# Performance work log

Measured on AMD Instinct MI355X. Metric: run time of the kernel, lower is better.

The kernel has to match this reference:

```python
import jax, jax.numpy as jnp
import numpy as np

OBS, HOR, PD, HID, NH, PROTO = 8, 8, 128, 256, 8, 32
B, N = 8, 4096

def _gelu(x):
    return jax.nn.gelu(x, approximate=False)  # torch nn.GELU default is exact erf

def setup_inputs():
    key = jax.random.key(0)
    ks = iter(jax.random.split(key, 40))
    nrm = lambda shape, s=0.02: jax.random.normal(next(ks), shape, dtype=jnp.float32) * s
    return {
        'obs_points': jax.random.normal(next(ks), (B, N, OBS, 2), dtype=jnp.float32),
        'obs_vis': jax.random.randint(next(ks), (B, N, OBS), 0, 2).astype(bool),
        'rel_xy': jax.random.normal(next(ks), (B, N, 2), dtype=jnp.float32),
        'anchor_obs': jax.random.normal(next(ks), (B, OBS, 2), dtype=jnp.float32),
        'anchor_obs_vel': jax.random.normal(next(ks), (B, OBS, 2), dtype=jnp.float32),
        'semantic_feat': jax.random.normal(next(ks), (B, N, 10), dtype=jnp.float32),
        'ln_w': jnp.ones((OBS * 7,), jnp.float32),
        'ln_b': jnp.zeros((OBS * 7,), jnp.float32),
        'enc_w1': nrm((OBS * 7, PD)), 'enc_b1': jnp.zeros((PD,), jnp.float32),
        'enc_w2': nrm((PD, PD)), 'enc_b2': jnp.zeros((PD,), jnp.float32),
        'time_embed': nrm((HOR, HID)),
        'anchor_w': nrm((OBS * 4, HID)), 'anchor_b': jnp.zeros((HID,), jnp.float32),
        'query_w': nrm((PD, HID)), 'query_b': jnp.zeros((HID,), jnp.float32),
        'in_proj_w': nrm((HID, 3 * HID)), 'in_proj_b': jnp.zeros((3 * HID,), jnp.float32),
        'out_proj_w': nrm((HID, HID)), 'out_proj_b': jnp.zeros((HID,), jnp.float32),
        'ah_w': nrm((HID, 2)), 'ah_b': jnp.zeros((2,), jnp.float32),
        'rh_w1': nrm((HID + PD + 2, HID)), 'rh_b1': jnp.zeros((HID,), jnp.float32),
        'rh_w2': nrm((HID, 2)), 'rh_b2': jnp.zeros((2,), jnp.float32),
        'vh_w1': nrm((HID + PD, HID // 2)), 'vh_b1': jnp.zeros((HID // 2,), jnp.float32),
        'vh_w2': nrm((HID // 2, 1)), 'vh_b2': jnp.zeros((1,), jnp.float32),
        'sh_w': nrm((HID, PROTO)), 'sh_b': jnp.zeros((PROTO,), jnp.float32),
    }

def reference(obs_points, obs_vis, rel_xy, anchor_obs, anchor_obs_vel, semantic_feat,
              ln_w, ln_b, enc_w1, enc_b1, enc_w2, enc_b2, time_embed,
              anchor_w, anchor_b, query_w, query_b, in_proj_w, in_proj_b,
              out_proj_w, out_proj_b, ah_w, ah_b, rh_w1, rh_b1, rh_w2, rh_b2,
              vh_w1, vh_b1, vh_w2, vh_b2, sh_w, sh_b):
    del semantic_feat  # unused, matches original
    Bc, Nc, T, _ = obs_points.shape
    # ---- PointTraceEncoder ----
    vel = jnp.concatenate([jnp.zeros_like(obs_points[:, :, :1]),
                           obs_points[:, :, 1:] - obs_points[:, :, :-1]], axis=2)
    rel = jnp.broadcast_to(rel_xy[:, :, None, :], (Bc, Nc, T, 2))
    feat = jnp.concatenate([obs_points, vel, obs_vis.astype(jnp.float32)[..., None], rel],
                           axis=-1).reshape(Bc, Nc, T * 7)
    mu = feat.mean(-1, keepdims=True)
    var = ((feat - mu) ** 2).mean(-1, keepdims=True)
    x = (feat - mu) / jnp.sqrt(var + 1e-5) * ln_w + ln_b
    point_tokens = _gelu(_gelu(x @ enc_w1 + enc_b1) @ enc_w2 + enc_b2)  # [B,N,PD]
    # ---- queries / memory ----
    anchor_feat = jnp.concatenate([anchor_obs, anchor_obs_vel], -1).reshape(Bc, -1)
    tq = time_embed[None] + (anchor_feat @ anchor_w + anchor_b)[:, None]  # [B,HOR,HID]
    mem = point_tokens @ query_w + query_b  # [B,N,HID]
    # ---- multi-head cross attention ----
    D = tq.shape[-1]; dh = D // NH
    q = tq @ in_proj_w[:, :D] + in_proj_b[:D]
    k = mem @ in_proj_w[:, D:2 * D] + in_proj_b[D:2 * D]
    v = mem @ in_proj_w[:, 2 * D:] + in_proj_b[2 * D:]
    qh = q.reshape(Bc, -1, NH, dh).transpose(0, 2, 1, 3)
    kh = k.reshape(Bc, -1, NH, dh).transpose(0, 2, 1, 3)
    vh = v.reshape(Bc, -1, NH, dh).transpose(0, 2, 1, 3)
    attn = jax.nn.softmax(jnp.einsum('bhqd,bhkd->bhqk', qh, kh) / jnp.sqrt(jnp.float32(dh)), axis=-1)
    o = jnp.einsum('bhqk,bhkd->bhqd', attn, vh).transpose(0, 2, 1, 3).reshape(Bc, -1, D)
    future = o @ out_proj_w + out_proj_b  # [B,HOR,HID]
    # ---- heads ----
    last_anchor = anchor_obs[:, -1]
    anchor_delta = 0.1 * jnp.tanh(future @ ah_w + ah_b)
    anchor_pred = last_anchor[:, None] + jnp.cumsum(anchor_delta, axis=1)  # [B,HOR,2]
    Hq = future.shape[1]
    ft_e = jnp.broadcast_to(future[:, :, None, :], (Bc, Hq, Nc, D))
    pt_e = jnp.broadcast_to(point_tokens[:, None], (Bc, Hq, Nc, point_tokens.shape[-1]))
    rel_e = jnp.broadcast_to(rel_xy[:, None], (Bc, Hq, Nc, 2))
    per_point = jnp.concatenate([ft_e, pt_e, rel_e], axis=-1)  # [B,HOR,N,HID+PD+2]
    residual = 0.1 * jnp.tanh(_gelu(per_point @ rh_w1 + rh_b1) @ rh_w2 + rh_b2)
    pred_points = anchor_pred[:, :, None, :] + residual
    vis_logits = (_gelu(per_point[..., :-2] @ vh_w1 + vh_b1) @ vh_w2 + vh_b2)[..., 0]
    sem_logits = future @ sh_w + sh_b
    return (anchor_pred,
            pred_points.transpose(0, 2, 1, 3),   # [B,N,HOR,2]
            vis_logits.transpose(0, 2, 1),       # [B,N,HOR]
            sem_logits)                           # [B,HOR,PROTO]
```

## Files before the change

kernel.cpp:

```cpp
#include <hip/hip_runtime.h>
#include <math.h>

#define BB 8
#define NN 4096
#define TT 8
#define HORQ 8
#define PD 128
#define HID 256
#define NHD 8
#define DH 32
#define FE 56
#define NC 8
#define CH 512

typedef __attribute__((ext_vector_type(8))) short short8;
typedef __attribute__((ext_vector_type(4))) float floatx4;

__device__ __forceinline__ float gelu_fast(float x) {
    float x2 = x * x;
    float y2 = x * fmaf(0.0713551f, x2, 1.5957691f);
    float e = __expf(y2);
    return x - x * __builtin_amdgcn_rcpf(1.f + e);
}

__device__ __forceinline__ short f2b(float x) {
    union { float f; unsigned u; } c; c.f = x;
    unsigned r = c.u + 0x7fffu + ((c.u >> 16) & 1u);
    return (short)(r >> 16);
}

__global__ __launch_bounds__(256) void k_fuse(
    const float* __restrict__ qw, const float* __restrict__ qb,
    const float* __restrict__ ipw, const float* __restrict__ ipb,
    float* __restrict__ Wk, float* __restrict__ Wv,
    float* __restrict__ bk, float* __restrict__ bv)
{
    int j = threadIdx.x;
    int blk = blockIdx.x;
    if (blk < PD) {
        float sk = 0.f, sv = 0.f;
        for (int l = 0; l < HID; l++) {
            float w = qw[blk * HID + l];
            sk += w * ipw[l * 768 + 256 + j];
            sv += w * ipw[l * 768 + 512 + j];
        }
        Wk[blk * HID + j] = sk;
        Wv[blk * HID + j] = sv;
    } else {
        float sk = ipb[256 + j], sv = ipb[512 + j];
        for (int l = 0; l < HID; l++) {
            float w = qb[l];
            sk += w * ipw[l * 768 + 256 + j];
            sv += w * ipw[l * 768 + 512 + j];
        }
        bk[j] = sk;
        bv[j] = sv;
    }
}

__global__ __launch_bounds__(256) void k_prep(
    const float* __restrict__ Wk, const float* __restrict__ Wv,
    const float* __restrict__ rw1, const float* __restrict__ vw1,
    const float* __restrict__ w1, const float* __restrict__ w2,
    short* __restrict__ Wfrag, short* __restrict__ w1frag, short* __restrict__ w2frag)
{
    int tid = threadIdx.x;
    int blk = blockIdx.x;
    int ks = tid >> 6, lane = tid & 63;
    int quad = lane >> 4, c16 = lane & 15;
    if (blk < 56) {
        int nt = blk;
        int n = nt * 16 + c16;
        for (int j = 0; j < 8; j++) {
            int k = ks * 32 + quad * 8 + j;
            float v;
            if (n < 256)      v = Wk[k * HID + n];
            else if (n < 512) v = Wv[k * HID + (n - 256)];
            else if (n < 768) v = rw1[(256 + k) * HID + (n - 512)];
            else              v = vw1[(256 + k) * PD + (n - 768)];
            Wfrag[((nt * 4 + ks) * 64 + lane) * 8 + j] = f2b(v);
        }
    } else if (blk < 64) {
        if (ks < 2) {
            int nt = blk - 56;
            int n = nt * 16 + c16;
            for (int j = 0; j < 8; j++) {
                int k = ks * 32 + quad * 8 + j;
                float v = (k < FE) ? w1[k * PD + n] : 0.f;
                w1frag[((nt * 2 + ks) * 64 + lane) * 8 + j] = f2b(v);
            }
        }
    } else {
        int nt = blk - 64;
        int n = nt * 16 + c16;
        for (int j = 0; j < 8; j++) {
            int k = ks * 32 + quad * 8 + j;
            w2frag[((nt * 4 + ks) * 64 + lane) * 8 + j] = f2b(w2[k * PD + n]);
        }
    }
}

#define U1_OFF 0
#define XNB_OFF 17408
#define PTB_OFF 26624
#define RXY_OFF 44032
#define MU_OFF 44544
#define RS_OFF 44800
#define SMEM_BYTES 45056

__global__ __launch_bounds__(256) void k_main(
    const float* __restrict__ obs, const int* __restrict__ vis,
    const float* __restrict__ rel,
    const float* __restrict__ lnw, const float* __restrict__ lnb,
    const float* __restrict__ b1, const float* __restrict__ b2,
    const short* __restrict__ Wfrag, const short* __restrict__ w1frag,
    const short* __restrict__ w2frag,
    const float* __restrict__ bk, const float* __restrict__ bv,
    const float* __restrict__ rw1,
    float* __restrict__ kb, float* __restrict__ vb,
    float* __restrict__ P1, float* __restrict__ P2)
{
    __shared__ __align__(16) char smem[SMEM_BYTES];
    float* xnf = (float*)(smem + U1_OFF);
    short* h1b = (short*)(smem + U1_OFF);
    short* xnb = (short*)(smem + XNB_OFF);
    short* ptb = (short*)(smem + PTB_OFF);
    float* rxyS = (float*)(smem + RXY_OFF);
    float* muS = (float*)(smem + MU_OFF);
    float* rsS = (float*)(smem + RS_OFF);

    int tid = threadIdx.x;
    int w = tid >> 6, lane = tid & 63;
    int quad = lane >> 4, c16 = lane & 15;
    int bn0 = blockIdx.x * 64;

    for (int idx = tid; idx < 64 * FE; idx += 256) {
        int p = idx / FE, e = idx - p * FE;
        int t = e / 7, c = e - t * 7;
        int bn = bn0 + p;
        float v;
        if (c < 2)       v = obs[(bn * TT + t) * 2 + c];
        else if (c < 4)  v = (t == 0) ? 0.f : (obs[(bn * TT + t) * 2 + (c - 2)] - obs[(bn * TT + t - 1) * 2 + (c - 2)]);
        else if (c == 4) v = (float)vis[bn * TT + t];
        else             v = rel[bn * 2 + (c - 5)];
        xnf[p * 57 + e] = v;
    }
    if (tid < 128) rxyS[tid] = rel[bn0 * 2 + tid];
    __syncthreads();

    if (tid < 64) {
        float s = 0.f, ss = 0.f;
        for (int e = 0; e < FE; e++) { float v = xnf[tid * 57 + e]; s += v; ss += v * v; }
        float mu = s * (1.f / FE);
        float var = ss * (1.f / FE) - mu * mu;
        muS[tid] = mu;
        rsS[tid] = rsqrtf(var + 1e-5f);
    }
    __syncthreads();

    for (int idx = tid; idx < 64 * 64; idx += 256) {
        int p = idx >> 6, e = idx & 63;
        float v = 0.f;
        if (e < FE) v = (xnf[p * 57 + e] - muS[p]) * rsS[p] * lnw[e] + lnb[e];
        xnb[p * 72 + e] = f2b(v);
    }
    __syncthreads();

    {
        short8 af1[4][2];
        #pragma unroll
        for (int mt = 0; mt < 4; mt++)
            #pragma unroll
            for (int ks = 0; ks < 2; ks++)
                af1[mt][ks] = *(const short8*)(xnb + (mt * 16 + c16) * 72 + ks * 32 + quad * 8);
        #pragma unroll
        for (int ntl = 0; ntl < 2; ntl++) {
            int nt = w * 2 + ntl;
            short8 bf1[2];
            #pragma unroll
            for (int ks = 0; ks < 2; ks++)
                bf1[ks] = *(const short8*)(w1frag + ((nt * 2 + ks) * 64 + lane) * 8);
            int col = nt * 16 + c16;
            float bb = b1[col];
            #pragma unroll
            for (int mt = 0; mt < 4; mt++) {
                floatx4 acc = {0.f, 0.f, 0.f, 0.f};
                acc = __builtin_amdgcn_mfma_f32_16x16x32_bf16(af1[mt][0], bf1[0], acc, 0, 0, 0);
                acc = __builtin_amdgcn_mfma_f32_16x16x32_bf16(af1[mt][1], bf1[1], acc, 0, 0, 0);
                #pragma unroll
                for (int r = 0; r < 4; r++) {
                    int row = mt * 16 + quad * 4 + r;
                    h1b[row * 136 + col] = f2b(gelu_fast(acc[r] + bb));
                }
            }
        }
    }
    __syncthreads();

    {
        short8 af2[4][4];
        #pragma unroll
        for (int mt = 0; mt < 4; mt++)
            #pragma unroll
            for (int ks = 0; ks < 4; ks++)
                af2[mt][ks] = *(const short8*)(h1b + (mt * 16 + c16) * 136 + ks * 32 + quad * 8);
        #pragma unroll
        for (int ntl = 0; ntl < 2; ntl++) {
            int nt = w * 2 + ntl;
            short8 bf2[4];
            #pragma unroll
            for (int ks = 0; ks < 4; ks++)
                bf2[ks] = *(const short8*)(w2frag + ((nt * 4 + ks) * 64 + lane) * 8);
            int col = nt * 16 + c16;
            float bb = b2[col];
            #pragma unroll
            for (int mt = 0; mt < 4; mt++) {
                floatx4 acc = {0.f, 0.f, 0.f, 0.f};
                #pragma unroll
                for (int ks = 0; ks < 4; ks++)
                    acc = __builtin_amdgcn_mfma_f32_16x16x32_bf16(af2[mt][ks], bf2[ks], acc, 0, 0, 0);
                #pragma unroll
                for (int r = 0; r < 4; r++) {
                    int row = mt * 16 + quad * 4 + r;
                    ptb[row * 136 + col] = f2b(gelu_fast(acc[r] + bb));
                }
            }
        }
    }
    __syncthreads();

    {
        short8 af[4][4];
        #pragma unroll
        for (int mt = 0; mt < 4; mt++)
            #pragma unroll
            for (int ks = 0; ks < 4; ks++)
                af[mt][ks] = *(const short8*)(ptb + (mt * 16 + c16) * 136 + ks * 32 + quad * 8);
        for (int i = 0; i < 14; i++) {
            int nt = w + i * 4;
            short8 bf[4];
            #pragma unroll
            for (int ks = 0; ks < 4; ks++)
                bf[ks] = *(const short8*)(Wfrag + ((nt * 4 + ks) * 64 + lane) * 8);
            floatx4 acc[4];
            #pragma unroll
            for (int mt = 0; mt < 4; mt++) {
                acc[mt] = (floatx4){0.f, 0.f, 0.f, 0.f};
                #pragma unroll
                for (int ks = 0; ks < 4; ks++)
                    acc[mt] = __builtin_amdgcn_mfma_f32_16x16x32_bf16(af[mt][ks], bf[ks], acc[mt], 0, 0, 0);
            }
            int n = nt * 16 + c16;
            if (nt < 16) {
                float bb = bk[n];
                #pragma unroll
                for (int mt = 0; mt < 4; mt++)
                    #pragma unroll
                    for (int r = 0; r < 4; r++) {
                        int row = mt * 16 + quad * 4 + r;
                        kb[(size_t)(bn0 + row) * HID + n] = acc[mt][r] + bb;
                    }
            } else if (nt < 32) {
                int j = n - 256;
                float bb = bv[j];
                #pragma unroll
                for (int mt = 0; mt < 4; mt++)
                    #pragma unroll
                    for (int r = 0; r < 4; r++) {
                        int row = mt * 16 + quad * 4 + r;
                        vb[(size_t)(bn0 + row) * HID + j] = acc[mt][r] + bb;
                    }
            } else if (nt < 48) {
                int j = n - 512;
                float wr0 = rw1[384 * HID + j], wr1 = rw1[385 * HID + j];
                #pragma unroll
                for (int mt = 0; mt < 4; mt++)
                    #pragma unroll
                    for (int r = 0; r < 4; r++) {
                        int row = mt * 16 + quad * 4 + r;
                        P1[(size_t)(bn0 + row) * HID + j] =
                            acc[mt][r] + rxyS[row * 2] * wr0 + rxyS[row * 2 + 1] * wr1;
                    }
            } else {
                int j = n - 768;
                #pragma unroll
                for (int mt = 0; mt < 4; mt++)
                    #pragma unroll
                    for (int r = 0; r < 4; r++) {
                        int row = mt * 16 + quad * 4 + r;
                        P2[(size_t)(bn0 + row) * PD + j] = acc[mt][r];
                    }
            }
        }
    }
}

__global__ __launch_bounds__(256) void k_tq(
    const float* __restrict__ aobs, const float* __restrict__ avel,
    const float* __restrict__ te, const float* __restrict__ aw, const float* __restrict__ ab,
    const float* __restrict__ ipw, const float* __restrict__ ipb,
    float* __restrict__ qb_)
{
    __shared__ float af[32];
    __shared__ float tq[HID];
    int tid = threadIdx.x;
    int b = blockIdx.x >> 3, h = blockIdx.x & 7;
    if (tid < 32) {
        int t = tid >> 2, m = tid & 3;
        af[tid] = (m < 2) ? aobs[(b * TT + t) * 2 + m] : avel[(b * TT + t) * 2 + (m - 2)];
    }
    __syncthreads();
    float s = te[h * HID + tid] + ab[tid];
    for (int i = 0; i < 32; i++) s += af[i] * aw[i * HID + tid];
    tq[tid] = s;
    __syncthreads();
    float qv = ipb[tid];
    for (int i = 0; i < HID; i++) qv += tq[i] * ipw[i * 768 + tid];
    qb_[(size_t)blockIdx.x * HID + tid] = qv;
}

__global__ __launch_bounds__(256) void k_att(
    const float* __restrict__ qbuf, const float* __restrict__ kb, const float* __restrict__ vbuf,
    float* __restrict__ pm, float* __restrict__ pl, float* __restrict__ po)
{
    __shared__ float qs[8][DH];
    __shared__ float sc[8][CH];
    __shared__ float pos[8][8][DH];
    int tid = threadIdx.x;
    int bidx = blockIdx.x;
    int c = bidx & (NC - 1);
    int head = (bidx >> 3) & 7;
    int b = bidx >> 6;
    qs[tid >> 5][tid & 31] = qbuf[(size_t)(b * HORQ + (tid >> 5)) * HID + head * DH + (tid & 31)];
    __syncthreads();
    const float scale = 0.17677669529663688110f;
    for (int nn = tid; nn < CH; nn += 256) {
        int n = c * CH + nn;
        const float* kp = kb + (size_t)(b * NN + n) * HID + head * DH;
        float kr[DH];
        #pragma unroll
        for (int u = 0; u < DH; u += 4) {
            float4 f = *reinterpret_cast<const float4*>(kp + u);
            kr[u] = f.x; kr[u + 1] = f.y; kr[u + 2] = f.z; kr[u + 3] = f.w;
        }
        #pragma unroll
        for (int qq = 0; qq < 8; qq++) {
            float s = 0.f;
            #pragma unroll
            for (int d = 0; d < DH; d++) s += qs[qq][d] * kr[d];
            sc[qq][nn] = s * scale;
        }
    }
    __syncthreads();
    int qq = tid >> 5, r = tid & 31;
    float mx = -1e30f;
    for (int nn = r; nn < CH; nn += 32) mx = fmaxf(mx, sc[qq][nn]);
    #pragma unroll
    for (int m = 16; m; m >>= 1) mx = fmaxf(mx, __shfl_xor(mx, m, 32));
    float sum = 0.f;
    for (int nn = r; nn < CH; nn += 32) { float e = __expf(sc[qq][nn] - mx); sc[qq][nn] = e; sum += e; }
    #pragma unroll
    for (int m = 16; m; m >>= 1) sum += __shfl_xor(sum, m, 32);
    if (r == 0) { pm[bidx * 8 + qq] = mx; pl[bidx * 8 + qq] = sum; }
    __syncthreads();
    {
        int g = tid >> 5, d = tid & 31;
        float oacc[8];
        #pragma unroll
        for (int q2 = 0; q2 < 8; q2++) oacc[q2] = 0.f;
        const float* vp = vbuf + ((size_t)(b * NN + c * CH + g * 64)) * HID + head * DH + d;
        for (int i = 0; i < 64; i++) {
            float v = vp[(size_t)i * HID];
            int nn = g * 64 + i;
            #pragma unroll
            for (int q2 = 0; q2 < 8; q2++) oacc[q2] += sc[q2][nn] * v;
        }
        #pragma unroll
        for (int q2 = 0; q2 < 8; q2++) pos[g][q2][d] = oacc[q2];
    }
    __syncthreads();
    {
        int q2 = tid >> 5, d = tid & 31;
        float o = 0.f;
        #pragma unroll
        for (int gg = 0; gg < 8; gg++) o += pos[gg][q2][d];
        po[(size_t)(bidx * 8 + q2) * DH + d] = o;
    }
}

__global__ __launch_bounds__(256) void k_attc(
    const float* __restrict__ pm, const float* __restrict__ pl, const float* __restrict__ po,
    float* __restrict__ ob)
{
    int tid = threadIdx.x;
    int bh = blockIdx.x;
    int b = bh >> 3, head = bh & 7;
    int qq = tid >> 5, d = tid & 31;
    float M = -1e30f;
    for (int c = 0; c < NC; c++) M = fmaxf(M, pm[(bh * NC + c) * 8 + qq]);
    float L = 0.f, o = 0.f;
    for (int c = 0; c < NC; c++) {
        float w = __expf(pm[(bh * NC + c) * 8 + qq] - M);
        L += w * pl[(bh * NC + c) * 8 + qq];
        o += w * po[(size_t)((bh * NC + c) * 8 + qq) * DH + d];
    }
    ob[(size_t)(b * HORQ + qq) * HID + head * DH + d] = o / L;
}

__global__ __launch_bounds__(256) void k_fut(
    const float* __restrict__ ob, const float* __restrict__ opw, const float* __restrict__ opb,
    const float* __restrict__ rw1, const float* __restrict__ rb1,
    const float* __restrict__ vw1, const float* __restrict__ vb1,
    const float* __restrict__ shw, const float* __restrict__ shb,
    const float* __restrict__ ahw, const float* __restrict__ ahb,
    float* __restrict__ F1, float* __restrict__ F2, float* __restrict__ dl, float* __restrict__ sem)
{
    __shared__ float orow[HID], fut[HID];
    int tid = threadIdx.x;
    int bh = blockIdx.x;
    orow[tid] = ob[(size_t)bh * HID + tid];
    __syncthreads();
    float s = opb[tid];
    for (int i = 0; i < HID; i++) s += orow[i] * opw[i * HID + tid];
    fut[tid] = s;
    __syncthreads();
    float f1 = rb1[tid];
    for (int i = 0; i < HID; i++) f1 += fut[i] * rw1[i * HID + tid];
    F1[(size_t)bh * HID + tid] = f1;
    if (tid < PD) {
        float f2 = vb1[tid];
        for (int i = 0; i < HID; i++) f2 += fut[i] * vw1[i * PD + tid];
        F2[(size_t)bh * PD + tid] = f2;
    }
    if (tid < 32) {
        float s3 = shb[tid];
        for (int i = 0; i < HID; i++) s3 += fut[i] * shw[i * 32 + tid];
        sem[bh * 32 + tid] = s3;
    }
    if (tid < 2) {
        float a = ahb[tid];
        for (int i = 0; i < HID; i++) a += fut[i] * ahw[i * 2 + tid];
        dl[bh * 2 + tid] = 0.1f * tanhf(a);
    }
}

__global__ void k_cum(const float* __restrict__ aobs, const float* __restrict__ dl, float* __restrict__ out0)
{
    int tid = threadIdx.x;
    if (tid < 16) {
        int b = tid >> 1, c = tid & 1;
        float acc = aobs[(b * TT + 7) * 2 + c];
        for (int h = 0; h < HORQ; h++) {
            acc += dl[(b * HORQ + h) * 2 + c];
            out0[(b * HORQ + h) * 2 + c] = acc;
        }
    }
}

__global__ __launch_bounds__(256) void k_fin(
    const float* __restrict__ F1, const float* __restrict__ F2,
    const float* __restrict__ P1, const float* __restrict__ P2,
    const float* __restrict__ rw2, const float* __restrict__ rb2,
    const float* __restrict__ vw2, const float* __restrict__ vb2,
    const float* __restrict__ ap,
    float* __restrict__ out1, float* __restrict__ out2)
{
    int tid = threadIdx.x;
    int wv = tid >> 6;
    int half = (tid >> 5) & 1;
    int l = tid & 31;
    size_t bn = (size_t)blockIdx.x * 8 + wv * 2 + half;
    int b = (int)(bn >> 12);
    float p1r[8], w20[8], w21[8];
    #pragma unroll
    for (int u = 0; u < 8; u++) {
        int j = l + 32 * u;
        p1r[u] = P1[bn * HID + j];
        w20[u] = rw2[j * 2];
        w21[u] = rw2[j * 2 + 1];
    }
    float p2r[4], wv2r[4];
    #pragma unroll
    for (int u = 0; u < 4; u++) {
        int j = l + 32 * u;
        p2r[u] = P2[bn * PD + j];
        wv2r[u] = vw2[j];
    }
    float rb20 = rb2[0], rb21 = rb2[1], vb20 = vb2[0];
    for (int h = 0; h < HORQ; h++) {
        const float* f1p = F1 + (size_t)(b * HORQ + h) * HID;
        const float* f2p = F2 + (size_t)(b * HORQ + h) * PD;
        float s0 = 0.f, s1 = 0.f, sv = 0.f;
        #pragma unroll
        for (int u = 0; u < 8; u++) {
            float g = gelu_fast(f1p[l + 32 * u] + p1r[u]);
            s0 += g * w20[u];
            s1 += g * w21[u];
        }
        #pragma unroll
        for (int u = 0; u < 4; u++) {
            float g = gelu_fast(f2p[l + 32 * u] + p2r[u]);
            sv += g * wv2r[u];
        }
        #pragma unroll
        for (int m = 16; m; m >>= 1) {
            s0 += __shfl_xor(s0, m);
            s1 += __shfl_xor(s1, m);
            sv += __shfl_xor(sv, m);
        }
        if (l == 0) {
            float rx = 0.1f * tanhf(s0 + rb20);
            float ry = 0.1f * tanhf(s1 + rb21);
            out1[(bn * HORQ + h) * 2 + 0] = ap[(b * HORQ + h) * 2 + 0] + rx;
            out1[(bn * HORQ + h) * 2 + 1] = ap[(b * HORQ + h) * 2 + 1] + ry;
            out2[bn * HORQ + h] = sv + vb20;
        }
    }
}

extern "C" void kernel_launch(void* const* d_in, const int* in_sizes, int n_in,
                              void* d_out, int out_size, void* d_ws, size_t ws_size,
                              hipStream_t stream)
{
    const float* obs  = (const float*)d_in[0];
    const int*   vis  = (const int*)d_in[1];
    const float* rel  = (const float*)d_in[2];
    const float* aobs = (const float*)d_in[3];
    const float* avel = (const float*)d_in[4];
    const float* lnw = (const float*)d_in[6];
    const float* lnb = (const float*)d_in[7];
    const float* ew1 = (const float*)d_in[8];
    const float* eb1 = (const float*)d_in[9];
    const float* ew2 = (const float*)d_in[10];
    const float* eb2 = (const float*)d_in[11];
    const float* te  = (const float*)d_in[12];
    const float* aw  = (const float*)d_in[13];
    const float* ab  = (const float*)d_in[14];
    const float* qw  = (const float*)d_in[15];
    const float* qbias = (const float*)d_in[16];
    const float* ipw = (const float*)d_in[17];
    const float* ipb = (const float*)d_in[18];
    const float* opw = (const float*)d_in[19];
    const float* opb = (const float*)d_in[20];
    const float* ahw = (const float*)d_in[21];
    const float* ahb = (const float*)d_in[22];
    const float* rw1 = (const float*)d_in[23];
    const float* rb1 = (const float*)d_in[24];
    const float* rw2 = (const float*)d_in[25];
    const float* rb2 = (const float*)d_in[26];
    const float* vw1 = (const float*)d_in[27];
    const float* vb1 = (const float*)d_in[28];
    const float* vw2 = (const float*)d_in[29];
    const float* vb2 = (const float*)d_in[30];
    const float* shw = (const float*)d_in[31];
    const float* shb = (const float*)d_in[32];

    float* W = (float*)d_ws;
    size_t o = 0;
    float* Wk  = W + o; o += (size_t)PD * HID;
    float* Wv  = W + o; o += (size_t)PD * HID;
    float* bk  = W + o; o += HID;
    float* bv  = W + o; o += HID;
    float* qb_ = W + o; o += (size_t)BB * HORQ * HID;
    float* F1  = W + o; o += (size_t)BB * HORQ * HID;
    float* F2  = W + o; o += (size_t)BB * HORQ * PD;
    float* dl  = W + o; o += (size_t)BB * HORQ * 2;
    float* ob  = W + o; o += (size_t)BB * HORQ * HID;
    float* pm  = W + o; o += 512 * 8;
    float* pl  = W + o; o += 512 * 8;
    float* po  = W + o; o += (size_t)512 * 8 * DH;
    float* kb  = W + o; o += (size_t)BB * NN * HID;
    float* vbuf= W + o; o += (size_t)BB * NN * HID;
    float* P1  = W + o; o += (size_t)BB * NN * HID;
    float* P2  = W + o; o += (size_t)BB * NN * PD;
    short* Sf = (short*)(W + o);
    short* Wfrag  = Sf;
    short* w1frag = Sf + 114688;
    short* w2frag = Sf + 114688 + 8192;

    float* out0 = (float*)d_out;
    float* out1 = out0 + BB * HORQ * 2;
    float* out2 = out1 + (size_t)BB * NN * HORQ * 2;
    float* out3 = out2 + (size_t)BB * NN * HORQ;

    k_fuse<<<PD + 1, 256, 0, stream>>>(qw, qbias, ipw, ipb, Wk, Wv, bk, bv);
    k_prep<<<72, 256, 0, stream>>>(Wk, Wv, rw1, vw1, ew1, ew2, Wfrag, w1frag, w2frag);
    k_main<<<BB * NN / 64, 256, 0, stream>>>(obs, vis, rel, lnw, lnb, eb1, eb2,
                                             Wfrag, w1frag, w2frag, bk, bv, rw1,
                                             kb, vbuf, P1, P2);
    k_tq<<<BB * HORQ, 256, 0, stream>>>(aobs, avel, te, aw, ab, ipw, ipb, qb_);
    k_att<<<BB * NHD * NC, 256, 0, stream>>>(qb_, kb, vbuf, pm, pl, po);
    k_attc<<<BB * NHD, 256, 0, stream>>>(pm, pl, po, ob);
    k_fut<<<BB * HORQ, 256, 0, stream>>>(ob, opw, opb, rw1, rb1, vw1, vb1, shw, shb, ahw, ahb,
                                         F1, F2, dl, out3);
    k_cum<<<1, 64, 0, stream>>>(aobs, dl, out0);
    k_fin<<<BB * NN / 8, 256, 0, stream>>>(F1, F2, P1, P2, rw2, rb2, vw2, vb2, out0, out1, out2);
}
```

Measured before the change: 290.0 us.

## Store per-point projections as bf16, retile final head kernel, split attention finer

The per-point P1/P2 projections are now written in bf16 instead of fp32, halving their write and read traffic. The final head kernel is restructured so each thread owns one point and four horizons, reads packed bf16 vectors, accumulates without cross-lane shuffles, uses a fast tanh, and writes float4 outputs. Attention now uses 16 chunks of 256 keys instead of 8 of 512, which gives more blocks. The cost is bf16 rounding of the projections and per-thread uncoalesced strided row reads in the head kernel.

```diff
diff --git a/kernel.cpp b/kernel.cpp
--- a/kernel.cpp
+++ b/kernel.cpp
@@ -10,11 +10,12 @@
 #define NHD 8
 #define DH 32
 #define FE 56
-#define NC 8
-#define CH 512
+#define NC2 16
+#define CH2 256
 
 typedef __attribute__((ext_vector_type(8))) short short8;
 typedef __attribute__((ext_vector_type(4))) float floatx4;
+typedef unsigned short ushort_t;
 
 __device__ __forceinline__ float gelu_fast(float x) {
     float x2 = x * x;
@@ -23,10 +24,19 @@
     return x - x * __builtin_amdgcn_rcpf(1.f + e);
 }
 
-__device__ __forceinline__ short f2b(float x) {
+__device__ __forceinline__ float tanh_fast(float x) {
+    float e = __expf(2.f * x);
+    return 1.f - 2.f * __builtin_amdgcn_rcpf(1.f + e);
+}
+
+__device__ __forceinline__ ushort_t f2b(float x) {
     union { float f; unsigned u; } c; c.f = x;
     unsigned r = c.u + 0x7fffu + ((c.u >> 16) & 1u);
-    return (short)(r >> 16);
+    return (ushort_t)(r >> 16);
+}
+__device__ __forceinline__ float b2f(unsigned hi) {
+    union { unsigned u; float f; } c; c.u = hi;
+    return c.f;
 }
 
 __global__ __launch_bounds__(256) void k_fuse(
@@ -78,7 +88,7 @@
             else if (n < 512) v = Wv[k * HID + (n - 256)];
             else if (n < 768) v = rw1[(256 + k) * HID + (n - 512)];
             else              v = vw1[(256 + k) * PD + (n - 768)];
-            Wfrag[((nt * 4 + ks) * 64 + lane) * 8 + j] = f2b(v);
+            Wfrag[((nt * 4 + ks) * 64 + lane) * 8 + j] = (short)f2b(v);
         }
     } else if (blk < 64) {
         if (ks < 2) {
@@ -87,7 +97,7 @@
             for (int j = 0; j < 8; j++) {
                 int k = ks * 32 + quad * 8 + j;
                 float v = (k < FE) ? w1[k * PD + n] : 0.f;
-                w1frag[((nt * 2 + ks) * 64 + lane) * 8 + j] = f2b(v);
+                w1frag[((nt * 2 + ks) * 64 + lane) * 8 + j] = (short)f2b(v);
             }
         }
     } else {
@@ -95,7 +105,7 @@
         int n = nt * 16 + c16;
         for (int j = 0; j < 8; j++) {
             int k = ks * 32 + quad * 8 + j;
-            w2frag[((nt * 4 + ks) * 64 + lane) * 8 + j] = f2b(w2[k * PD + n]);
+            w2frag[((nt * 4 + ks) * 64 + lane) * 8 + j] = (short)f2b(w2[k * PD + n]);
         }
     }
 }
@@ -118,7 +128,7 @@
     const float* __restrict__ bk, const float* __restrict__ bv,
     const float* __restrict__ rw1,
     float* __restrict__ kb, float* __restrict__ vb,
-    float* __restrict__ P1, float* __restrict__ P2)
+    ushort_t* __restrict__ P1, ushort_t* __restrict__ P2)
 {
     __shared__ __align__(16) char smem[SMEM_BYTES];
     float* xnf = (float*)(smem + U1_OFF);
@@ -162,7 +172,7 @@
         int p = idx >> 6, e = idx & 63;
         float v = 0.f;
         if (e < FE) v = (xnf[p * 57 + e] - muS[p]) * rsS[p] * lnw[e] + lnb[e];
-        xnb[p * 72 + e] = f2b(v);
+        xnb[p * 72 + e] = (short)f2b(v);
     }
     __syncthreads();
 
@@ -190,7 +200,7 @@
                 #pragma unroll
                 for (int r = 0; r < 4; r++) {
                     int row = mt * 16 + quad * 4 + r;
-                    h1b[row * 136 + col] = f2b(gelu_fast(acc[r] + bb));
+                    h1b[row * 136 + col] = (short)f2b(gelu_fast(acc[r] + bb));
                 }
             }
         }
@@ -222,7 +232,7 @@
                 #pragma unroll
                 for (int r = 0; r < 4; r++) {
                     int row = mt * 16 + quad * 4 + r;
-                    ptb[row * 136 + col] = f2b(gelu_fast(acc[r] + bb));
+                    ptb[row * 136 + col] = (short)f2b(gelu_fast(acc[r] + bb));
                 }
             }
         }
@@ -279,7 +289,7 @@
                     for (int r = 0; r < 4; r++) {
                         int row = mt * 16 + quad * 4 + r;
                         P1[(size_t)(bn0 + row) * HID + j] =
-                            acc[mt][r] + rxyS[row * 2] * wr0 + rxyS[row * 2 + 1] * wr1;
+                            f2b(acc[mt][r] + rxyS[row * 2] * wr0 + rxyS[row * 2 + 1] * wr1);
                     }
             } else {
                 int j = n - 768;
@@ -288,7 +298,7 @@
                     #pragma unroll
                     for (int r = 0; r < 4; r++) {
                         int row = mt * 16 + quad * 4 + r;
-                        P2[(size_t)(bn0 + row) * PD + j] = acc[mt][r];
+                        P2[(size_t)(bn0 + row) * PD + j] = f2b(acc[mt][r]);
                     }
             }
         }
@@ -324,18 +334,19 @@
     float* __restrict__ pm, float* __restrict__ pl, float* __restrict__ po)
 {
     __shared__ float qs[8][DH];
-    __shared__ float sc[8][CH];
+    __shared__ float sc[8][CH2];
     __shared__ float pos[8][8][DH];
     int tid = threadIdx.x;
     int bidx = blockIdx.x;
-    int c = bidx & (NC - 1);
-    int head = (bidx >> 3) & 7;
-    int b = bidx >> 6;
+    int c = bidx & (NC2 - 1);
+    int head = (bidx >> 4) & 7;
+    int b = bidx >> 7;
     qs[tid >> 5][tid & 31] = qbuf[(size_t)(b * HORQ + (tid >> 5)) * HID + head * DH + (tid & 31)];
     __syncthreads();
     const float scale = 0.17677669529663688110f;
-    for (int nn = tid; nn < CH; nn += 256) {
-        int n = c * CH + nn;
+    {
+        int nn = tid;
+        int n = c * CH2 + nn;
         const float* kp = kb + (size_t)(b * NN + n) * HID + head * DH;
         float kr[DH];
         #pragma unroll
@@ -354,11 +365,13 @@
     __syncthreads();
     int qq = tid >> 5, r = tid & 31;
     float mx = -1e30f;
-    for (int nn = r; nn < CH; nn += 32) mx = fmaxf(mx, sc[qq][nn]);
+    #pragma unroll
+    for (int nn = r; nn < CH2; nn += 32) mx = fmaxf(mx, sc[qq][nn]);
     #pragma unroll
     for (int m = 16; m; m >>= 1) mx = fmaxf(mx, __shfl_xor(mx, m, 32));
     float sum = 0.f;
-    for (int nn = r; nn < CH; nn += 32) { float e = __expf(sc[qq][nn] - mx); sc[qq][nn] = e; sum += e; }
+    #pragma unroll
+    for (int nn = r; nn < CH2; nn += 32) { float e = __expf(sc[qq][nn] - mx); sc[qq][nn] = e; sum += e; }
     #pragma unroll
     for (int m = 16; m; m >>= 1) sum += __shfl_xor(sum, m, 32);
     if (r == 0) { pm[bidx * 8 + qq] = mx; pl[bidx * 8 + qq] = sum; }
@@ -368,10 +381,10 @@
         float oacc[8];
         #pragma unroll
         for (int q2 = 0; q2 < 8; q2++) oacc[q2] = 0.f;
-        const float* vp = vbuf + ((size_t)(b * NN + c * CH + g * 64)) * HID + head * DH + d;
-        for (int i = 0; i < 64; i++) {
+        const float* vp = vbuf + ((size_t)(b * NN + c * CH2 + g * 32)) * HID + head * DH + d;
+        for (int i = 0; i < 32; i++) {
             float v = vp[(size_t)i * HID];
-            int nn = g * 64 + i;
+            int nn = g * 32 + i;
             #pragma unroll
             for (int q2 = 0; q2 < 8; q2++) oacc[q2] += sc[q2][nn] * v;
         }
@@ -397,12 +410,12 @@
     int b = bh >> 3, head = bh & 7;
     int qq = tid >> 5, d = tid & 31;
     float M = -1e30f;
-    for (int c = 0; c < NC; c++) M = fmaxf(M, pm[(bh * NC + c) * 8 + qq]);
+    for (int c = 0; c < NC2; c++) M = fmaxf(M, pm[(bh * NC2 + c) * 8 + qq]);
     float L = 0.f, o = 0.f;
-    for (int c = 0; c < NC; c++) {
-        float w = __expf(pm[(bh * NC + c) * 8 + qq] - M);
-        L += w * pl[(bh * NC + c) * 8 + qq];
-        o += w * po[(size_t)((bh * NC + c) * 8 + qq) * DH + d];
+    for (int c = 0; c < NC2; c++) {
+        float w = __expf(pm[(bh * NC2 + c) * 8 + qq] - M);
+        L += w * pl[(bh * NC2 + c) * 8 + qq];
+        o += w * po[(size_t)((bh * NC2 + c) * 8 + qq) * DH + d];
     }
     ob[(size_t)(b * HORQ + qq) * HID + head * DH + d] = o / L;
 }
@@ -459,63 +472,92 @@
 
 __global__ __launch_bounds__(256) void k_fin(
     const float* __restrict__ F1, const float* __restrict__ F2,
-    const float* __restrict__ P1, const float* __restrict__ P2,
+    const ushort_t* __restrict__ P1, const ushort_t* __restrict__ P2,
     const float* __restrict__ rw2, const float* __restrict__ rb2,
     const float* __restrict__ vw2, const float* __restrict__ vb2,
     const float* __restrict__ ap,
     float* __restrict__ out1, float* __restrict__ out2)
 {
-    int tid = threadIdx.x;
-    int wv = tid >> 6;
-    int half = (tid >> 5) & 1;
-    int l = tid & 31;
-    size_t bn = (size_t)blockIdx.x * 8 + wv * 2 + half;
-    int b = (int)(bn >> 12);
-    float p1r[8], w20[8], w21[8];
+    int tile = blockIdx.x >> 1;
+    int hh = blockIdx.x & 1;
+    int h0 = hh * 4;
+    int bn = tile * 256 + threadIdx.x;
+    int b = bn >> 12;
+
+    const uint4* p1v = (const uint4*)(P1 + (size_t)bn * HID);
+    const uint4* p2v = (const uint4*)(P2 + (size_t)bn * PD);
+    const float* f1base = F1 + (size_t)(b * HORQ + h0) * HID;
+    const float* f2base = F2 + (size_t)(b * HORQ + h0) * PD;
+
+    float acc0[4], acc1[4], accv[4];
     #pragma unroll
-    for (int u = 0; u < 8; u++) {
-        int j = l + 32 * u;
-        p1r[u] = P1[bn * HID + j];
-        w20[u] = rw2[j * 2];
-        w21[u] = rw2[j * 2 + 1];
-    }
-    float p2r[4], wv2r[4];
+    for (int hi = 0; hi < 4; hi++) { acc0[hi] = 0.f; acc1[hi] = 0.f; accv[hi] = 0.f; }
+
+    for (int c = 0; c < 32; c++) {
+        uint4 q = p1v[c];
+        unsigned wd[4] = {q.x, q.y, q.z, q.w};
+        float p1f[8];
+        #pragma unroll
+        for (int u = 0; u < 4; u++) {
+            p1f[2 * u]     = b2f(wd[u] << 16);
+            p1f[2 * u + 1] = b2f(wd[u] & 0xffff0000u);
+        }
+        float w0[8], w1[8];
+        #pragma unroll
+        for (int u = 0; u < 8; u++) {
+            int j = c * 8 + u;
+            w0[u] = rw2[j * 2];
+            w1[u] = rw2[j * 2 + 1];
+        }
+        #pragma unroll
+        for (int hi = 0; hi < 4; hi++) {
+            const float* f1p = f1base + hi * HID + c * 8;
+            #pragma unroll
+            for (int u = 0; u < 8; u++) {
+                float g = gelu_fast(f1p[u] + p1f[u]);
+                acc0[hi] += g * w0[u];
+                acc1[hi] += g * w1[u];
+            }
+        }
+    }
+    for (int c = 0; c < 16; c++) {
+        uint4 q = p2v[c];
+        unsigned wd[4] = {q.x, q.y, q.z, q.w};
+        float p2f[8];
+        #pragma unroll
+        for (int u = 0; u < 4; u++) {
+            p2f[2 * u]     = b2f(wd[u] << 16);
+            p2f[2 * u + 1] = b2f(wd[u] & 0xffff0000u);
+        }
+        float wv[8];
+        #pragma unroll
+        for (int u = 0; u < 8; u++) wv[u] = vw2[c * 8 + u];
+        #pragma unroll
+        for (int hi = 0; hi < 4; hi++) {
+            const float* f2p = f2base + hi * PD + c * 8;
+            #pragma unroll
+            for (int u = 0; u < 8; u++) {
+                float g = gelu_fast(f2p[u] + p2f[u]);
+                accv[hi] += g * wv[u];
+            }
+        }
+    }
+
+    float rb20 = rb2[0], rb21 = rb2[1], vb20 = vb2[0];
+    float o1[8], o2[4];
     #pragma unroll
-    for (int u = 0; u < 4; u++) {
-        int j = l + 32 * u;
-        p2r[u] = P2[bn * PD + j];
-        wv2r[u] = vw2[j];
-    }
-    float rb20 = rb2[0], rb21 = rb2[1], vb20 = vb2[0];
-    for (int h = 0; h < HORQ; h++) {
-        const float* f1p = F1 + (size_t)(b * HORQ + h) * HID;
-        const float* f2p = F2 + (size_t)(b * HORQ + h) * PD;
-        float s0 = 0.f, s1 = 0.f, sv = 0.f;
-        #pragma unroll
-        for (int u = 0; u < 8; u++) {
-            float g = gelu_fast(f1p[l + 32 * u] + p1r[u]);
-            s0 += g * w20[u];
-            s1 += g * w21[u];
-        }
-        #pragma unroll
-        for (int u = 0; u < 4; u++) {
-            float g = gelu_fast(f2p[l + 32 * u] + p2r[u]);
-            sv += g * wv2r[u];
-        }
-        #pragma unroll
-        for (int m = 16; m; m >>= 1) {
-            s0 += __shfl_xor(s0, m);
-            s1 += __shfl_xor(s1, m);
-            sv += __shfl_xor(sv, m);
-        }
-        if (l == 0) {
-            float rx = 0.1f * tanhf(s0 + rb20);
-            float ry = 0.1f * tanhf(s1 + rb21);
-            out1[(bn * HORQ + h) * 2 + 0] = ap[(b * HORQ + h) * 2 + 0] + rx;
-            out1[(bn * HORQ + h) * 2 + 1] = ap[(b * HORQ + h) * 2 + 1] + ry;
-            out2[bn * HORQ + h] = sv + vb20;
-        }
-    }
+    for (int hi = 0; hi < 4; hi++) {
+        int h = h0 + hi;
+        float rx = 0.1f * tanh_fast(acc0[hi] + rb20);
+        float ry = 0.1f * tanh_fast(acc1[hi] + rb21);
+        o1[2 * hi]     = ap[(b * HORQ + h) * 2 + 0] + rx;
+        o1[2 * hi + 1] = ap[(b * HORQ + h) * 2 + 1] + ry;
+        o2[hi] = accv[hi] + vb20;
+    }
+    float4* o1p = (float4*)(out1 + ((size_t)bn * HORQ + h0) * 2);
+    o1p[0] = make_float4(o1[0], o1[1], o1[2], o1[3]);
+    o1p[1] = make_float4(o1[4], o1[5], o1[6], o1[7]);
+    *(float4*)(out2 + (size_t)bn * HORQ + h0) = make_float4(o2[0], o2[1], o2[2], o2[3]);
 }
 
 extern "C" void kernel_launch(void* const* d_in, const int* in_sizes, int n_in,
@@ -566,13 +608,13 @@
     float* F2  = W + o; o += (size_t)BB * HORQ * PD;
     float* dl  = W + o; o += (size_t)BB * HORQ * 2;
     float* ob  = W + o; o += (size_t)BB * HORQ * HID;
-    float* pm  = W + o; o += 512 * 8;
-    float* pl  = W + o; o += 512 * 8;
-    float* po  = W + o; o += (size_t)512 * 8 * DH;
+    float* pm  = W + o; o += (size_t)BB * NHD * NC2 * 8;
+    float* pl  = W + o; o += (size_t)BB * NHD * NC2 * 8;
+    float* po  = W + o; o += (size_t)BB * NHD * NC2 * 8 * DH;
     float* kb  = W + o; o += (size_t)BB * NN * HID;
     float* vbuf= W + o; o += (size_t)BB * NN * HID;
-    float* P1  = W + o; o += (size_t)BB * NN * HID;
-    float* P2  = W + o; o += (size_t)BB * NN * PD;
+    ushort_t* P1 = (ushort_t*)(W + o); o += (size_t)BB * NN * HID / 2;
+    ushort_t* P2 = (ushort_t*)(W + o); o += (size_t)BB * NN * PD / 2;
     short* Sf = (short*)(W + o);
     short* Wfrag  = Sf;
     short* w1frag = Sf + 114688;
@@ -589,10 +631,11 @@
                                              Wfrag, w1frag, w2frag, bk, bv, rw1,
                                              kb, vbuf, P1, P2);
     k_tq<<<BB * HORQ, 256, 0, stream>>>(aobs, avel, te, aw, ab, ipw, ipb, qb_);
-    k_att<<<BB * NHD * NC, 256, 0, stream>>>(qb_, kb, vbuf, pm, pl, po);
+    k_att<<<BB * NHD * NC2, 256, 0, stream>>>(qb_, kb, vbuf, pm, pl, po);
     k_attc<<<BB * NHD, 256, 0, stream>>>(pm, pl, po, ob);
     k_fut<<<BB * HORQ, 256, 0, stream>>>(ob, opw, opb, rw1, rb1, vw1, vb1, shw, shb, ahw, ahb,
                                          F1, F2, dl, out3);
     k_cum<<<1, 64, 0, stream>>>(aobs, dl, out0);
-    k_fin<<<BB * NN / 8, 256, 0, stream>>>(F1, F2, P1, P2, rw2, rb2, vw2, vb2, out0, out1, out2);
-}
+    k_fin<<<(BB * NN / 256) * 2, 256, 0, stream>>>(F1, F2, P1, P2, rw2, rb2, vw2, vb2,
+                                                   out0, out1, out2);
+}
```

New measurement: 290.3 us. About the same (+0.1%).
